# Optimization experiments

Hardware: AMD Instinct MI355X
Metric: run time of the kernel (lower is better)

## Reference

```python
import jax, jax.numpy as jnp
import numpy as np

N_NODE = 2048   # n_node
N_TIME = 10     # t / look_back
STEP_K = 5
PROB_C = 0.98
LN_EPS = 1e-5


def setup_inputs() -> dict:
    key = jax.random.key(0)
    k1, k2 = jax.random.split(key, 2)
    # dynamic adjacency-like input: [n_node, n_time, n_node], nonnegative
    x = jax.random.uniform(k1, (N_NODE, N_TIME, N_NODE), dtype=jnp.float32)
    # learned restart weights, init = prob_c (already in [0,1])
    weight = jnp.full((N_TIME, STEP_K), PROB_C, dtype=jnp.float32)
    # LayerNorm(n_node) params
    ln_gamma = jnp.ones((N_NODE,), dtype=jnp.float32)
    ln_beta = jnp.zeros((N_NODE,), dtype=jnp.float32)
    return {"x": x, "weight": weight, "ln_gamma": ln_gamma, "ln_beta": ln_beta}


def _layer_norm(h, gamma, beta):
    mu = jnp.mean(h, axis=-1, keepdims=True)
    var = jnp.mean((h - mu) ** 2, axis=-1, keepdims=True)
    return (h - mu) * jax.lax.rsqrt(var + LN_EPS) * gamma + beta


def reference(x, weight, ln_gamma, ln_beta):
    # x: [N, T, N]; weight: [T, K]
    w = jnp.clip(weight, 0.0, 1.0)
    n = x.shape[0]
    eye = jnp.eye(n, dtype=x.dtype)  # Pt0

    G = jnp.transpose(x, (1, 0, 2))                 # [T, N, N]
    deg = jnp.sum(G, axis=-1, keepdims=True) + 1e-8  # row degree
    G_norm = G / deg                                # D^{-1} G (row-normalize)

    def per_time(Gt_norm, wt):
        # random walk with restart, accumulate sum of P over K steps
        def step(carry, wi):
            P, acc = carry
            Pc = wi * (P @ Gt_norm) + (1.0 - wi) * eye
            return (Pc, acc + Pc), None
        (_, final_P), _ = jax.lax.scan(step, (eye, jnp.zeros_like(eye)), wt)
        return _layer_norm(final_P, ln_gamma, ln_beta)

    out = jax.vmap(per_time)(G_norm, w)  # [T, N, N]
    return jnp.transpose(out, (1, 0, 2))  # [N, T, N]
```

## Files before the change

kernel.cpp:

```cpp
#include <hip/hip_runtime.h>
#include <stdint.h>

#define NN 2048
#define TT 10
#define KST 5
#define BK 64
#define NKT2 (NN / BK)

typedef float f32x4 __attribute__((ext_vector_type(4)));
typedef __bf16 bf16x8 __attribute__((ext_vector_type(8)));
typedef unsigned short u16x8 __attribute__((ext_vector_type(8)));

using as3_void = __attribute__((address_space(3))) void;
using as1_const_void = const __attribute__((address_space(1))) void;

__device__ __forceinline__ unsigned short f2bf_bits(float f) {
    unsigned u = __builtin_bit_cast(unsigned, f);
    unsigned r = u + 0x7FFFu + ((u >> 16) & 1u);
    return (unsigned short)(r >> 16);
}
__device__ __forceinline__ float bf2f(unsigned short b) {
    return __builtin_bit_cast(float, ((unsigned)b) << 16);
}

__global__ __launch_bounds__(256) void deg_kernel(const float* __restrict__ x,
                                                  float* __restrict__ deg) {
    const int i = blockIdx.x;
    const int t = blockIdx.y;
    const int tid = threadIdx.x;
    const float4* r4 = (const float4*)(x + ((size_t)i * TT + t) * NN);
    float4 a = r4[tid];
    float4 b = r4[tid + 256];
    float s = a.x + a.y + a.z + a.w + b.x + b.y + b.z + b.w;
    #pragma unroll
    for (int m = 32; m >= 1; m >>= 1) s += __shfl_xor(s, m, 64);
    __shared__ float red[4];
    if ((tid & 63) == 0) red[tid >> 6] = s;
    __syncthreads();
    if (tid == 0) deg[(size_t)t * NN + i] = red[0] + red[1] + red[2] + red[3] + 1e-8f;
}

__global__ __launch_bounds__(256) void gnt_init_kernel(const float* __restrict__ x,
                                                       const float* __restrict__ deg,
                                                       const float* __restrict__ w,
                                                       unsigned short* __restrict__ gnt,
                                                       unsigned short* __restrict__ p1,
                                                       int t0) {
    const int tl = blockIdx.z;
    const int t  = t0 + tl;
    float w0 = w[t * KST + 0];
    w0 = fminf(fmaxf(w0, 0.0f), 1.0f);
    const float om = 1.0f - w0;
    const int n0 = blockIdx.x * 64;
    const int k0 = blockIdx.y * 64;
    __shared__ float tile[64][65];
    const int tx = threadIdx.x & 63;
    const int ty = threadIdx.x >> 6;
    unsigned short* p1dst = p1 + (size_t)tl * NN * NN;
    #pragma unroll
    for (int p = 0; p < 16; ++p) {
        int kr = p * 4 + ty;
        float rd = 1.0f / deg[(size_t)t * NN + k0 + kr];
        float v = x[(((size_t)(k0 + kr)) * TT + t) * NN + n0 + tx] * rd;
        tile[kr][tx] = v;
        float pv = w0 * v + ((k0 + kr) == (n0 + tx) ? om : 0.0f);
        p1dst[(size_t)(k0 + kr) * NN + n0 + tx] = f2bf_bits(pv);
    }
    __syncthreads();
    unsigned short* dst = gnt + (size_t)tl * NN * NN;
    #pragma unroll
    for (int p = 0; p < 16; ++p) {
        int nr = p * 4 + ty;
        dst[(size_t)(n0 + nr) * NN + k0 + tx] = f2bf_bits(tile[tx][nr]);
    }
}

#define FENCE __asm__ volatile("" ::: "memory")

#define MFMA_PHASE(PA, PB)                                                        \
  do {                                                                            \
    __builtin_amdgcn_s_setprio(1);                                                \
    _Pragma("unroll")                                                             \
    for (int f_ = 0; f_ < 4; ++f_) {                                              \
      _Pragma("unroll")                                                           \
      for (int g_ = 0; g_ < 2; ++g_) {                                            \
        acc[(PA)*4 + f_][(PB)*2 + g_] = __builtin_amdgcn_mfma_f32_16x16x32_bf16(  \
            af[f_][0], bfr[g_][0], acc[(PA)*4 + f_][(PB)*2 + g_], 0, 0, 0);       \
        acc[(PA)*4 + f_][(PB)*2 + g_] = __builtin_amdgcn_mfma_f32_16x16x32_bf16(  \
            af[f_][1], bfr[g_][1], acc[(PA)*4 + f_][(PB)*2 + g_], 0, 0, 0);       \
      }                                                                           \
    }                                                                             \
    __builtin_amdgcn_s_setprio(0);                                                \
  } while (0)

__global__ __launch_bounds__(512, 2) void gemm_step256(
        const unsigned short* __restrict__ Pprev,
        const unsigned short* __restrict__ gnt,
        const float* __restrict__ w,
        unsigned short* __restrict__ Pnext,
        int t0, int kstep) {
    extern __shared__ char smem[];

    const int nwg  = (int)gridDim.x;
    const int flat = (int)blockIdx.x;
    const int xcd  = flat & 7;
    const int q    = nwg >> 3, r = nwg & 7;
    const int wgid = (xcd < r ? xcd * (q + 1) : r * (q + 1) + (xcd - r) * q) + (flat >> 3);
    const int tl   = wgid >> 6;
    const int s    = wgid & 63;
    const int g4   = s >> 2, w4 = s & 3;
    const int tm   = ((g4 >> 2) << 1) | (w4 >> 1);
    const int tn   = ((g4 & 3) << 1) | (w4 & 1);
    const int t    = t0 + tl;

    const int tid  = threadIdx.x;
    const int lane = tid & 63;
    const int wv   = tid >> 6;
    const int wm   = wv >> 2;
    const int wn   = wv & 3;
    const int lr   = lane & 15;
    const int quad = lane >> 4;
    const int swz  = lr & 7;

    const unsigned short* Ab = Pprev + (size_t)tl * NN * NN;
    const unsigned short* Bb = gnt   + (size_t)tl * NN * NN;

    const int srow  = lane >> 3;
    const int sslot = (lane & 7) ^ srow;
    const unsigned short* pa[2][2];
    const unsigned short* pb[2][2];
    #pragma unroll
    for (int h = 0; h < 2; ++h)
        #pragma unroll
        for (int l = 0; l < 2; ++l) {
            const int rA = tm * 256 + h * 128 + l * 64 + wv * 8 + srow;
            const int rB = tn * 256 + h * 128 + l * 64 + wv * 8 + srow;
            pa[h][l] = Ab + (size_t)rA * NN + sslot * 8;
            pb[h][l] = Bb + (size_t)rB * NN + sslot * 8;
        }

    auto stageA = [&](int kt, int b, int h) {
        #pragma unroll
        for (int l = 0; l < 2; ++l)
            __builtin_amdgcn_global_load_lds(
                (as1_const_void*)(pa[h][l] + kt * BK),
                (as3_void*)(smem + b * 65536 + h * 16384 + l * 8192 + wv * 1024),
                16, 0, 0);
    };
    auto stageB = [&](int kt, int b, int h) {
        #pragma unroll
        for (int l = 0; l < 2; ++l)
            __builtin_amdgcn_global_load_lds(
                (as1_const_void*)(pb[h][l] + kt * BK),
                (as3_void*)(smem + b * 65536 + 32768 + h * 16384 + l * 8192 + wv * 1024),
                16, 0, 0);
    };

    bf16x8 af[4][2];
    bf16x8 bfr[2][2];
    const int sA = ((quad)     ^ swz) * 16;
    const int sB = ((quad + 4) ^ swz) * 16;
    auto lda = [&](int b, int half) {
        const char* base = smem + b * 65536 + half * 16384 + (wm * 64 + lr) * 128;
        #pragma unroll
        for (int f = 0; f < 4; ++f) {
            af[f][0] = *(const bf16x8*)(base + f * 2048 + sA);
            af[f][1] = *(const bf16x8*)(base + f * 2048 + sB);
        }
    };
    auto ldb = [&](int b, int half) {
        const char* base = smem + b * 65536 + 32768 + half * 16384 + (wn * 32 + lr) * 128;
        #pragma unroll
        for (int g = 0; g < 2; ++g) {
            bfr[g][0] = *(const bf16x8*)(base + g * 2048 + sA);
            bfr[g][1] = *(const bf16x8*)(base + g * 2048 + sB);
        }
    };

    f32x4 acc[8][4];
    #pragma unroll
    for (int i = 0; i < 8; ++i)
        #pragma unroll
        for (int j = 0; j < 4; ++j)
            acc[i][j] = (f32x4){0.0f, 0.0f, 0.0f, 0.0f};

    stageA(0, 0, 0);
    stageB(0, 0, 0);
    stageB(0, 0, 1);
    stageA(0, 0, 1);

    for (int kt = 0; kt < NKT2 - 1; ++kt) {
        const int buf  = kt & 1;
        const int nbuf = buf ^ 1;
        FENCE; __builtin_amdgcn_s_waitcnt(0xF74); __builtin_amdgcn_s_barrier(); FENCE;
        lda(buf, 0);
        ldb(buf, 0);
        stageA(kt + 1, nbuf, 0);
        MFMA_PHASE(0, 0);
        FENCE; __builtin_amdgcn_s_barrier(); FENCE;
        FENCE; __builtin_amdgcn_s_waitcnt(0xF74); __builtin_amdgcn_s_barrier(); FENCE;
        ldb(buf, 1);
        stageB(kt + 1, nbuf, 0);
        MFMA_PHASE(0, 1);
        FENCE; __builtin_amdgcn_s_barrier(); FENCE;
        FENCE; __builtin_amdgcn_s_waitcnt(0xF74); __builtin_amdgcn_s_barrier(); FENCE;
        lda(buf, 1);
        stageB(kt + 1, nbuf, 1);
        MFMA_PHASE(1, 1);
        FENCE; __builtin_amdgcn_s_barrier(); FENCE;
        ldb(buf, 0);
        stageA(kt + 1, nbuf, 1);
        MFMA_PHASE(1, 0);
        FENCE; __builtin_amdgcn_s_barrier(); FENCE;
    }

    {
        const int buf = (NKT2 - 1) & 1;
        FENCE; __builtin_amdgcn_s_waitcnt(0xF74); __builtin_amdgcn_s_barrier(); FENCE;
        lda(buf, 0);
        ldb(buf, 0);
        MFMA_PHASE(0, 0);
        FENCE; __builtin_amdgcn_s_barrier(); FENCE;
        FENCE; __builtin_amdgcn_s_waitcnt(0xF72); __builtin_amdgcn_s_barrier(); FENCE;
        ldb(buf, 1);
        MFMA_PHASE(0, 1);
        FENCE; __builtin_amdgcn_s_barrier(); FENCE;
        FENCE; __builtin_amdgcn_s_waitcnt(0xF70); __builtin_amdgcn_s_barrier(); FENCE;
        lda(buf, 1);
        MFMA_PHASE(1, 1);
        ldb(buf, 0);
        MFMA_PHASE(1, 0);
    }

    float wk = w[t * KST + kstep];
    wk = fminf(fmaxf(wk, 0.0f), 1.0f);
    const float om = 1.0f - wk;
    unsigned short* __restrict__ Pn = Pnext + (size_t)tl * NN * NN;
    #pragma unroll
    for (int F = 0; F < 8; ++F) {
        const int mrow0 = tm * 256 + (F >> 2) * 128 + wm * 64 + (F & 3) * 16 + quad * 4;
        #pragma unroll
        for (int v = 0; v < 4; ++v) {
            const int m = mrow0 + v;
            const size_t mb = (size_t)m * NN;
            #pragma unroll
            for (int G = 0; G < 4; ++G) {
                const int n = tn * 256 + (G >> 1) * 128 + wn * 32 + (G & 1) * 16 + lr;
                float val = wk * acc[F][G][v] + (m == n ? om : 0.0f);
                Pn[mb + n] = f2bf_bits(val);
            }
        }
    }
}

__global__ __launch_bounds__(256) void ln_kernel(const unsigned short* __restrict__ Pall,
                                                 const float* __restrict__ gamma,
                                                 const float* __restrict__ beta,
                                                 float* __restrict__ out,
                                                 int t0, size_t strideK) {
    const int m  = blockIdx.x;
    const int tl = blockIdx.y;
    const int t  = t0 + tl;
    const int tid = threadIdx.x;
    const int j = tid * 8;

    const size_t rbase = (size_t)tl * NN * NN + (size_t)m * NN + j;
    float v[8] = {0, 0, 0, 0, 0, 0, 0, 0};
    #pragma unroll
    for (int k = 0; k < KST; ++k) {
        u16x8 pv = *(const u16x8*)(Pall + (size_t)k * strideK + rbase);
        #pragma unroll
        for (int e = 0; e < 8; ++e) v[e] += bf2f(pv[e]);
    }

    float s = 0.0f;
    #pragma unroll
    for (int e = 0; e < 8; ++e) s += v[e];
    #pragma unroll
    for (int mm = 32; mm >= 1; mm >>= 1) s += __shfl_xor(s, mm, 64);
    __shared__ float red[4];
    if ((tid & 63) == 0) red[tid >> 6] = s;
    __syncthreads();
    const float mu = (red[0] + red[1] + red[2] + red[3]) * (1.0f / NN);

    float q = 0.0f;
    float dx[8];
    #pragma unroll
    for (int e = 0; e < 8; ++e) { dx[e] = v[e] - mu; q += dx[e] * dx[e]; }
    __syncthreads();
    #pragma unroll
    for (int mm = 32; mm >= 1; mm >>= 1) q += __shfl_xor(q, mm, 64);
    if ((tid & 63) == 0) red[tid >> 6] = q;
    __syncthreads();
    const float var = (red[0] + red[1] + red[2] + red[3]) * (1.0f / NN);
    const float sc = rsqrtf(var + 1e-5f);

    float4 g0 = *(const float4*)(gamma + j);
    float4 g1 = *(const float4*)(gamma + j + 4);
    float4 b0 = *(const float4*)(beta + j);
    float4 b1 = *(const float4*)(beta + j + 4);
    const size_t ob = ((size_t)m * TT + t) * NN + j;
    float4 o0, o1;
    o0.x = dx[0] * sc * g0.x + b0.x;  o0.y = dx[1] * sc * g0.y + b0.y;
    o0.z = dx[2] * sc * g0.z + b0.z;  o0.w = dx[3] * sc * g0.w + b0.w;
    o1.x = dx[4] * sc * g1.x + b1.x;  o1.y = dx[5] * sc * g1.y + b1.y;
    o1.z = dx[6] * sc * g1.z + b1.z;  o1.w = dx[7] * sc * g1.w + b1.w;
    *(float4*)(out + ob)     = o0;
    *(float4*)(out + ob + 4) = o1;
}

extern "C" void kernel_launch(void* const* d_in, const int* in_sizes, int n_in,
                              void* d_out, int out_size, void* d_ws, size_t ws_size,
                              hipStream_t stream) {
    (void)in_sizes; (void)n_in; (void)out_size;
    const float* x     = (const float*)d_in[0];
    const float* w     = (const float*)d_in[1];
    const float* gamma = (const float*)d_in[2];
    const float* beta  = (const float*)d_in[3];
    float* out = (float*)d_out;

    static bool attr_done = false;
    if (!attr_done) {
        (void)hipFuncSetAttribute((const void*)gemm_step256,
                                  hipFuncAttributeMaxDynamicSharedMemorySize, 131072);
        attr_done = true;
    }

    char* ws = (char*)d_ws;
    float* deg = (float*)ws;
    size_t off = ((size_t)TT * NN * sizeof(float) + 255) & ~(size_t)255;
    const size_t per_t = (size_t)NN * NN * sizeof(unsigned short);
    size_t avail = ws_size > off ? ws_size - off : 0;
    int TB = (int)(avail / ((1 + KST) * per_t));
    if (TB < 1) TB = 1;
    if (TB > TT) TB = TT;
    unsigned short* gnt  = (unsigned short*)(ws + off);
    unsigned short* Pall = gnt + (size_t)TB * NN * NN;
    const size_t strideK = (size_t)TB * NN * NN;

    deg_kernel<<<dim3(NN, TT), 256, 0, stream>>>(x, deg);

    for (int t0 = 0; t0 < TT; t0 += TB) {
        const int tb = (TT - t0) < TB ? (TT - t0) : TB;
        gnt_init_kernel<<<dim3(32, 32, tb), 256, 0, stream>>>(x, deg, w, gnt, Pall, t0);
        for (int k = 2; k <= KST; ++k) {
            const unsigned short* Pp = Pall + (size_t)(k - 2) * strideK;
            unsigned short*       Pn = Pall + (size_t)(k - 1) * strideK;
            gemm_step256<<<dim3(64 * tb), 512, 131072, stream>>>(Pp, gnt, w, Pn, t0, k - 1);
        }
        ln_kernel<<<dim3(NN, tb), 256, 0, stream>>>(Pall, gamma, beta, out, t0, strideK);
    }
}
```

Measured before the change: 1.054 ms.

## Keep both B fragments in registers and cut barriers in GEMM main loop

Splits the B fragment registers into two sets, so the first B half loaded from LDS can be reused for the final MFMA phase instead of being reloaded. This drops one ldb per k-tile and removes several block barriers, reordering the async global-to-LDS stage issues and waitcnt values to match. It aims to reduce LDS traffic and synchronisation stalls. In exchange it raises register pressure under the 512x2 launch bound, and the new waitcnt/barrier ordering could introduce LDS hazards if the counts are wrong.

Result: slower. 1.078 ms (+2.3%).

```diff
diff --git a/kernel.cpp b/kernel.cpp
--- a/kernel.cpp
+++ b/kernel.cpp
@@ -77,20 +77,18 @@
 
 #define FENCE __asm__ volatile("" ::: "memory")
 
-#define MFMA_PHASE(PA, PB)                                                        \
+#define MFMA_PHASE(PA, PB, BARR)                                                  \
   do {                                                                            \
-    __builtin_amdgcn_s_setprio(1);                                                \
     _Pragma("unroll")                                                             \
     for (int f_ = 0; f_ < 4; ++f_) {                                              \
       _Pragma("unroll")                                                           \
       for (int g_ = 0; g_ < 2; ++g_) {                                            \
         acc[(PA)*4 + f_][(PB)*2 + g_] = __builtin_amdgcn_mfma_f32_16x16x32_bf16(  \
-            af[f_][0], bfr[g_][0], acc[(PA)*4 + f_][(PB)*2 + g_], 0, 0, 0);       \
+            af[f_][0], BARR[g_][0], acc[(PA)*4 + f_][(PB)*2 + g_], 0, 0, 0);      \
         acc[(PA)*4 + f_][(PB)*2 + g_] = __builtin_amdgcn_mfma_f32_16x16x32_bf16(  \
-            af[f_][1], bfr[g_][1], acc[(PA)*4 + f_][(PB)*2 + g_], 0, 0, 0);       \
+            af[f_][1], BARR[g_][1], acc[(PA)*4 + f_][(PB)*2 + g_], 0, 0, 0);      \
       }                                                                           \
     }                                                                             \
-    __builtin_amdgcn_s_setprio(0);                                                \
   } while (0)
 
 __global__ __launch_bounds__(512, 2) void gemm_step256(
@@ -157,7 +155,8 @@
     };
 
     bf16x8 af[4][2];
-    bf16x8 bfr[2][2];
+    bf16x8 bf0[2][2];
+    bf16x8 bf1[2][2];
     const int sA = ((quad)     ^ swz) * 16;
     const int sB = ((quad + 4) ^ swz) * 16;
     auto lda = [&](int b, int half) {
@@ -168,12 +167,12 @@
             af[f][1] = *(const bf16x8*)(base + f * 2048 + sB);
         }
     };
-    auto ldb = [&](int b, int half) {
+    auto ldb = [&](int b, int half, bf16x8 (&dst)[2][2]) {
         const char* base = smem + b * 65536 + 32768 + half * 16384 + (wn * 32 + lr) * 128;
         #pragma unroll
         for (int g = 0; g < 2; ++g) {
-            bfr[g][0] = *(const bf16x8*)(base + g * 2048 + sA);
-            bfr[g][1] = *(const bf16x8*)(base + g * 2048 + sB);
+            dst[g][0] = *(const bf16x8*)(base + g * 2048 + sA);
+            dst[g][1] = *(const bf16x8*)(base + g * 2048 + sB);
         }
     };
 
@@ -194,42 +193,46 @@
         const int nbuf = buf ^ 1;
         FENCE; __builtin_amdgcn_s_waitcnt(0xF74); __builtin_amdgcn_s_barrier(); FENCE;
         lda(buf, 0);
-        ldb(buf, 0);
+        ldb(buf, 0, bf0);
         stageA(kt + 1, nbuf, 0);
-        MFMA_PHASE(0, 0);
-        FENCE; __builtin_amdgcn_s_barrier(); FENCE;
-        FENCE; __builtin_amdgcn_s_waitcnt(0xF74); __builtin_amdgcn_s_barrier(); FENCE;
-        ldb(buf, 1);
         stageB(kt + 1, nbuf, 0);
-        MFMA_PHASE(0, 1);
-        FENCE; __builtin_amdgcn_s_barrier(); FENCE;
-        FENCE; __builtin_amdgcn_s_waitcnt(0xF74); __builtin_amdgcn_s_barrier(); FENCE;
+        __builtin_amdgcn_s_setprio(1);
+        MFMA_PHASE(0, 0, bf0);
+        __builtin_amdgcn_s_setprio(0);
+        FENCE; __builtin_amdgcn_s_waitcnt(0xF76); __builtin_amdgcn_s_barrier(); FENCE;
+        ldb(buf, 1, bf1);
+        stageB(kt + 1, nbuf, 1);
+        stageA(kt + 1, nbuf, 1);
+        __builtin_amdgcn_s_setprio(1);
+        MFMA_PHASE(0, 1, bf1);
+        __builtin_amdgcn_s_setprio(0);
+        FENCE; __builtin_amdgcn_s_waitcnt(0xF78); __builtin_amdgcn_s_barrier(); FENCE;
         lda(buf, 1);
-        stageB(kt + 1, nbuf, 1);
-        MFMA_PHASE(1, 1);
-        FENCE; __builtin_amdgcn_s_barrier(); FENCE;
-        ldb(buf, 0);
-        stageA(kt + 1, nbuf, 1);
-        MFMA_PHASE(1, 0);
-        FENCE; __builtin_amdgcn_s_barrier(); FENCE;
+        __builtin_amdgcn_s_setprio(1);
+        MFMA_PHASE(1, 1, bf1);
+        MFMA_PHASE(1, 0, bf0);
+        __builtin_amdgcn_s_setprio(0);
     }
 
     {
         const int buf = (NKT2 - 1) & 1;
         FENCE; __builtin_amdgcn_s_waitcnt(0xF74); __builtin_amdgcn_s_barrier(); FENCE;
         lda(buf, 0);
-        ldb(buf, 0);
-        MFMA_PHASE(0, 0);
-        FENCE; __builtin_amdgcn_s_barrier(); FENCE;
+        ldb(buf, 0, bf0);
+        __builtin_amdgcn_s_setprio(1);
+        MFMA_PHASE(0, 0, bf0);
+        __builtin_amdgcn_s_setprio(0);
         FENCE; __builtin_amdgcn_s_waitcnt(0xF72); __builtin_amdgcn_s_barrier(); FENCE;
-        ldb(buf, 1);
-        MFMA_PHASE(0, 1);
-        FENCE; __builtin_amdgcn_s_barrier(); FENCE;
+        ldb(buf, 1, bf1);
+        __builtin_amdgcn_s_setprio(1);
+        MFMA_PHASE(0, 1, bf1);
+        __builtin_amdgcn_s_setprio(0);
         FENCE; __builtin_amdgcn_s_waitcnt(0xF70); __builtin_amdgcn_s_barrier(); FENCE;
         lda(buf, 1);
-        MFMA_PHASE(1, 1);
-        ldb(buf, 0);
-        MFMA_PHASE(1, 0);
+        __builtin_amdgcn_s_setprio(1);
+        MFMA_PHASE(1, 1, bf1);
+        MFMA_PHASE(1, 0, bf0);
+        __builtin_amdgcn_s_setprio(0);
     }
 
     float wk = w[t * KST + kstep];
```
